# Performance work log

Hardware: AMD Instinct MI355X
Metric: run time of the kernel (lower is better)

## Reference

```python
import jax, jax.numpy as jnp
import numpy as np

EMBED = 128   # embed_dim
HEADS = 8
POINTS = 4
H_SP, W_SP = 51, 102   # hardcoded spatial_shapes in __init__
BEV = 100              # bev_res
HRES = 50              # height_res


def _make_ref_points():
    """Exact numpy replica of the spherical grid built in __init__."""
    eps = 1e-6
    x = np.linspace(-71 / 2, 71 / 2, BEV)
    y = np.linspace(-71 / 2, 71 / 2, BEV)
    z = np.linspace(-50 / 2, 50 / 2, HRES)
    gx, gy, gz = np.meshgrid(x, y, z, indexing='ij')
    phi = np.sign(gy + eps) * np.arccos(gx / (np.sqrt(gx ** 2 + gy ** 2) + eps))
    theta = np.arccos(gz / (np.sqrt(gx ** 2 + gy ** 2 + gz ** 2) + eps))
    phi = 2 * np.pi - phi
    phi[phi > 2 * np.pi] -= 2 * np.pi
    col = phi / (2 * np.pi)   # grd_col_cross
    row = theta / np.pi       # grd_row_cross
    ref = np.stack([col, row], axis=-1)              # (BEV, BEV, HRES, 2)
    ref = ref.transpose(2, 0, 1, 3).reshape(HRES, BEV * BEV, 2)
    return jnp.asarray(ref, dtype=jnp.float32)


def setup_inputs() -> dict:
    key = jax.random.key(0)
    ks = jax.random.split(key, 12)
    d = EMBED
    s = 0.02
    return {
        'query': jax.random.normal(ks[0], (1, BEV * BEV, d), jnp.float32),
        'value': jax.random.normal(ks[1], (1, H_SP * W_SP, d), jnp.float32),
        'ref_points': _make_ref_points(),
        'W_off': jax.random.normal(ks[2], (d, HEADS * POINTS * 2), jnp.float32) * s,
        'b_off': jax.random.normal(ks[3], (HEADS * POINTS * 2,), jnp.float32) * s,
        'W_attn': jax.random.normal(ks[4], (d, HEADS * POINTS), jnp.float32) * s,
        'b_attn': jax.random.normal(ks[5], (HEADS * POINTS,), jnp.float32) * s,
        'W_val': jax.random.normal(ks[6], (d, d), jnp.float32) * s,
        'b_val': jax.random.normal(ks[7], (d,), jnp.float32) * s,
        'W_out': jax.random.normal(ks[8], (d, d), jnp.float32) * s,
        'b_out': jax.random.normal(ks[9], (d,), jnp.float32) * s,
        'W_proj': jax.random.normal(ks[10], (d, 1), jnp.float32) * s,
        'b_proj': jax.random.normal(ks[11], (1,), jnp.float32) * s,
    }


def _bilinear_sample(vflat, loc):
    """grid_sample(bilinear, zero padding, align_corners=False).
    vflat: (B, H*W, hd) value maps; loc: (B, N, 2) normalized [0,1] (x,y)."""
    px = loc[..., 0] * W_SP - 0.5
    py = loc[..., 1] * H_SP - 0.5
    x0 = jnp.floor(px)
    y0 = jnp.floor(py)
    dx = (px - x0)[..., None]
    dy = (py - y0)[..., None]
    x0i = x0.astype(jnp.int32)
    y0i = y0.astype(jnp.int32)

    def gather(xi, yi):
        valid = (xi >= 0) & (xi < W_SP) & (yi >= 0) & (yi < H_SP)
        idx = jnp.clip(yi, 0, H_SP - 1) * W_SP + jnp.clip(xi, 0, W_SP - 1)
        v = jnp.take_along_axis(vflat, idx[..., None], axis=1)  # (B, N, hd)
        return v * valid[..., None].astype(vflat.dtype)

    v00 = gather(x0i, y0i)
    v01 = gather(x0i + 1, y0i)
    v10 = gather(x0i, y0i + 1)
    v11 = gather(x0i + 1, y0i + 1)
    return (v00 * (1 - dx) * (1 - dy) + v01 * dx * (1 - dy)
            + v10 * (1 - dx) * dy + v11 * dx * dy)


def reference(query, value, ref_points, W_off, b_off, W_attn, b_attn,
              W_val, b_val, W_out, b_out, W_proj, b_proj):
    bs, nq, d = query.shape
    hd = d // HEADS
    L = ref_points.shape[0]

    # query-dependent MSDA projections (identical across height levels)
    offsets = (query @ W_off + b_off).reshape(bs, nq, HEADS, POINTS, 2)
    aw = jax.nn.softmax((query @ W_attn + b_attn).reshape(bs, nq, HEADS, POINTS), axis=-1)
    awt = aw.transpose(0, 2, 1, 3)                              # (bs, heads, nq, points)
    v = (value @ W_val + b_val).reshape(bs, -1, HEADS, hd)
    vflat = v.transpose(0, 2, 1, 3).reshape(bs * HEADS, H_SP * W_SP, hd)
    norm = jnp.asarray([W_SP, H_SP], dtype=query.dtype)         # offset_normalizer [W, H]

    def per_level(ref):  # ref: (nq, 2) -> MSDA output with its internal residual
        loc = ref[None, :, None, None, :] + offsets / norm      # (bs, nq, heads, pts, 2)
        loc = loc.transpose(0, 2, 1, 3, 4).reshape(bs * HEADS, nq * POINTS, 2)
        samp = _bilinear_sample(vflat, loc).reshape(bs, HEADS, nq, POINTS, hd)
        out = jnp.einsum('bhnp,bhnpd->bnhd', awt, samp).reshape(bs, nq, d)
        return out @ W_out + b_out + query                      # mmcv MSDA adds identity

    grd = jax.vmap(per_level)(ref_points)                       # (L, bs, nq, d)
    grd_3d = grd.transpose(1, 2, 0, 3).reshape(bs, BEV, BEV, L, d)
    weights = jax.nn.softmax(grd_3d @ W_proj + b_proj, axis=3)  # (bs, BEV, BEV, L, 1)
    max_height_index = jnp.argmax(weights, axis=3)              # (bs, BEV, BEV, 1)
    grd_bev = (weights * grd_3d).sum(axis=3)                    # (bs, BEV, BEV, d)
    return grd_bev.reshape(bs, nq, d) + query, max_height_index
```

## Files before the change

### kernel.cpp

```cpp
#include <hip/hip_runtime.h>
#include <math.h>

#define EMBED   128
#define NHEADS  8
#define NPOINTS 4
#define HD      16
#define HSP     51
#define WSP     102
#define NPIX    (HSP * WSP)
#define NQ      10000
#define NLVL    50

#define GRID_A ((NPIX + 7) / 8)
#define GRID_B (NQ / 8)

__global__ __launch_bounds__(256) void k_prep(
    const float* __restrict__ value,
    const float* __restrict__ Wv,
    const float* __restrict__ bv,
    const float* __restrict__ query,
    const float* __restrict__ Woff,
    const float* __restrict__ boff,
    const float* __restrict__ Wattn,
    const float* __restrict__ battn,
    const float* __restrict__ Wout,
    const float* __restrict__ Wproj,
    float* __restrict__ vout,
    float* __restrict__ gout,
    float* __restrict__ off_out,
    float* __restrict__ aw_out) {
    const int b = blockIdx.x;
    const int t = threadIdx.x;
    __shared__ float srow[8][EMBED];
    __shared__ float4 u_s[32];

    if (b < GRID_A) {
        const int p   = t >> 5;
        const int s   = t & 31;
        const int pix = b * 8 + p;
        const int pl  = min(pix, NPIX - 1);
        *(float4*)&srow[p][s * 4] =
            *(const float4*)(value + (size_t)pl * EMBED + s * 4);
        if (t < 32) {
            float4 u4 = {0.f, 0.f, 0.f, 0.f};
            const float* w0 = Wout + (size_t)(t * 4 + 0) * EMBED;
            const float* w1 = Wout + (size_t)(t * 4 + 1) * EMBED;
            const float* w2 = Wout + (size_t)(t * 4 + 2) * EMBED;
            const float* w3 = Wout + (size_t)(t * 4 + 3) * EMBED;
#pragma unroll 4
            for (int d = 0; d < EMBED; d += 4) {
                const float4 wp = *(const float4*)(Wproj + d);
                const float4 a = *(const float4*)(w0 + d);
                const float4 c = *(const float4*)(w1 + d);
                const float4 e = *(const float4*)(w2 + d);
                const float4 f = *(const float4*)(w3 + d);
                u4.x = fmaf(a.x, wp.x, u4.x); u4.x = fmaf(a.y, wp.y, u4.x);
                u4.x = fmaf(a.z, wp.z, u4.x); u4.x = fmaf(a.w, wp.w, u4.x);
                u4.y = fmaf(c.x, wp.x, u4.y); u4.y = fmaf(c.y, wp.y, u4.y);
                u4.y = fmaf(c.z, wp.z, u4.y); u4.y = fmaf(c.w, wp.w, u4.y);
                u4.z = fmaf(e.x, wp.x, u4.z); u4.z = fmaf(e.y, wp.y, u4.z);
                u4.z = fmaf(e.z, wp.z, u4.z); u4.z = fmaf(e.w, wp.w, u4.z);
                u4.w = fmaf(f.x, wp.x, u4.w); u4.w = fmaf(f.y, wp.y, u4.w);
                u4.w = fmaf(f.z, wp.z, u4.w); u4.w = fmaf(f.w, wp.w, u4.w);
            }
            u_s[t] = u4;
        }
        __syncthreads();
        float4 acc = *(const float4*)(bv + s * 4);
        const float* vr = srow[p];
        const float* wp = Wv + s * 4;
#pragma unroll 8
        for (int k = 0; k < EMBED; ++k) {
            const float qv = vr[k];
            const float4 w4 = *(const float4*)(wp + (size_t)k * EMBED);
            acc.x = fmaf(qv, w4.x, acc.x);
            acc.y = fmaf(qv, w4.y, acc.y);
            acc.z = fmaf(qv, w4.z, acc.z);
            acc.w = fmaf(qv, w4.w, acc.w);
        }
        const float4 u4 = u_s[s];
        float gp = acc.x * u4.x;
        gp = fmaf(acc.y, u4.y, gp);
        gp = fmaf(acc.z, u4.z, gp);
        gp = fmaf(acc.w, u4.w, gp);
        gp += __shfl_xor(gp, 1, 64);
        gp += __shfl_xor(gp, 2, 64);
        if (pix < NPIX) {
            *(float4*)(vout + (size_t)pix * EMBED + s * 4) = acc;
            if ((s & 3) == 0)
                gout[(size_t)pix * NHEADS + (s >> 2)] = gp;
        }
    } else if (b < GRID_A + GRID_B) {
        const int qi = t >> 5;
        const int s  = t & 31;
        const int q  = (b - GRID_A) * 8 + qi;
        *(float4*)&srow[qi][s * 4] =
            *(const float4*)(query + (size_t)q * EMBED + s * 4);
        __syncthreads();
        if (s < 24) {
            const float* vr = srow[qi];
            const float* wp;
            int wstride;
            float4 acc;
            if (s < 16) {
                wp = Woff + s * 4; wstride = 64;
                acc = *(const float4*)(boff + s * 4);
            } else {
                wp = Wattn + (s - 16) * 4; wstride = 32;
                acc = *(const float4*)(battn + (s - 16) * 4);
            }
#pragma unroll 8
            for (int k = 0; k < EMBED; ++k) {
                const float qv = vr[k];
                const float4 w4 = *(const float4*)(wp + (size_t)k * wstride);
                acc.x = fmaf(qv, w4.x, acc.x);
                acc.y = fmaf(qv, w4.y, acc.y);
                acc.z = fmaf(qv, w4.z, acc.z);
                acc.w = fmaf(qv, w4.w, acc.w);
            }
            if (s < 16) {
                *(float4*)(off_out + (size_t)q * 64 + s * 4) = acc;
            } else {
                const float mx = fmaxf(fmaxf(acc.x, acc.y), fmaxf(acc.z, acc.w));
                const float e0 = __expf(acc.x - mx), e1 = __expf(acc.y - mx);
                const float e2 = __expf(acc.z - mx), e3 = __expf(acc.w - mx);
                const float inv = 1.f / (e0 + e1 + e2 + e3);
                float4 r;
                r.x = e0 * inv; r.y = e1 * inv; r.z = e2 * inv; r.w = e3 * inv;
                *(float4*)(aw_out + (size_t)q * 32 + (s - 16) * 4) = r;
            }
        }
    }
}

__global__ __launch_bounds__(256, 6) void k_main(
    const float* __restrict__ query,
    const float* __restrict__ refp,
    const float* __restrict__ voff,
    const float* __restrict__ vaw,
    const float* __restrict__ vflat,
    const float* __restrict__ gmap,
    const float* __restrict__ Wout,
    const float* __restrict__ bout,
    float* __restrict__ out0,
    float* __restrict__ out1) {
    const int t = threadIdx.x;
    const int qslot = t >> 7;
    const int w2 = (t >> 6) & 1;
    const int half = (t >> 5) & 1;
    const int sub = t & 31;
    const int h  = sub >> 2;
    const int c4 = sub & 3;
    const int q = blockIdx.x * 2 + qslot;

    __shared__ float  s_rpy[2][NLVL];
    __shared__ float4 s_acc[2][32];
    __shared__ float  s_z[2], s_m[2];
    __shared__ int    s_b[2];
    __shared__ float  s_e[2][2][2][13];

    if (t < 2 * NLVL) {
        const int ql = t / NLVL, l = t - ql * NLVL;
        const int qq = blockIdx.x * 2 + ql;
        s_rpy[ql][l] = refp[((size_t)l * NQ + qq) * 2 + 1];
    }

    const float4* offp = (const float4*)(voff + (size_t)q * 64 + h * 8);
    const float4 o01 = offp[0];
    const float4 o23 = offp[1];
    const float4 awv4 = *(const float4*)(vaw + (size_t)q * 32 + h * 4);
    const float rpx = refp[(size_t)q * 2];
    const float4* vbase = (const float4*)vflat + h * 4 + c4;

    const float offx[4] = {o01.x, o01.z, o23.x, o23.z};
    const float offy[4] = {o01.y, o01.w, o23.y, o23.w};
    const float awv[4]  = {awv4.x, awv4.y, awv4.z, awv4.w};

    float wx0[NPOINTS], wx1[NPOINTS], oyc[NPOINTS];
    int xo0[NPOINTS], xo1[NPOINTS];
#pragma unroll
    for (int p = 0; p < NPOINTS; ++p) {
        const float px = fmaf(rpx, (float)WSP, offx[p]) - 0.5f;
        const float fx = floorf(px);
        const float dx = px - fx;
        const int x0 = (int)fx, x1 = x0 + 1;
        const float a = awv[p];
        wx0[p] = ((unsigned)x0 < (unsigned)WSP) ? a * (1.f - dx) : 0.f;
        wx1[p] = ((unsigned)x1 < (unsigned)WSP) ? a * dx : 0.f;
        xo0[p] = min(max(x0, 0), WSP - 1) * 32;
        xo1[p] = min(max(x1, 0), WSP - 1) * 32;
        oyc[p] = offy[p] - 0.5f;
    }

    const float offx_c = (c4 == 0) ? o01.x : (c4 == 1) ? o01.z : (c4 == 2) ? o23.x : o23.z;
    const float offy_c = (c4 == 0) ? o01.y : (c4 == 1) ? o01.w : (c4 == 2) ? o23.y : o23.w;
    const float a_c    = (c4 == 0) ? awv4.x : (c4 == 1) ? awv4.y : (c4 == 2) ? awv4.z : awv4.w;
    const float pxc = fmaf(rpx, (float)WSP, offx_c) - 0.5f;
    const float fxc = floorf(pxc);
    const float dxc = pxc - fxc;
    const int x0c = (int)fxc, x1c = x0c + 1;
    const float gwx0 = ((unsigned)x0c < (unsigned)WSP) ? a_c * (1.f - dxc) : 0.f;
    const float gwx1 = ((unsigned)x1c < (unsigned)WSP) ? a_c * dxc : 0.f;
    const int gx0 = min(max(x0c, 0), WSP - 1) * NHEADS + h;
    const int gx1 = min(max(x1c, 0), WSP - 1) * NHEADS + h;
    const float oyc_c = offy_c - 0.5f;

    __syncthreads();

    const int niter = 13 - w2;
    float Z = 0.f, m = -1e30f;
    int best = 0;

#pragma unroll
    for (int i = 0; i < 13; ++i) {
        if (i >= niter) break;
        const int l = 4 * i + (w2 << 1) + half;
        const float rpy = s_rpy[qslot][l];
        const float py = fmaf(rpy, (float)HSP, oyc_c);
        const float fy = floorf(py);
        const float dy = py - fy;
        const int y0 = (int)fy, y1 = y0 + 1;
        const float t0 = ((unsigned)y0 < (unsigned)HSP) ? (1.f - dy) : 0.f;
        const float t1 = ((unsigned)y1 < (unsigned)HSP) ? dy : 0.f;
        const int r0 = min(max(y0, 0), HSP - 1) * (WSP * NHEADS);
        const int r1 = min(max(y1, 0), HSP - 1) * (WSP * NHEADS);
        const float g00 = gmap[r0 + gx0];
        const float g01 = gmap[r0 + gx1];
        const float g10 = gmap[r1 + gx0];
        const float g11 = gmap[r1 + gx1];
        float row0 = gwx0 * g00; row0 = fmaf(gwx1, g01, row0);
        float row1 = gwx0 * g10; row1 = fmaf(gwx1, g11, row1);
        float pg = t0 * row0; pg = fmaf(t1, row1, pg);
#pragma unroll
        for (int d = 1; d < 32; d <<= 1)
            pg += __shfl_xor(pg, d, 64);
        const float e = __expf(pg);
        Z += e;
        best = (pg > m) ? l : best;
        m = fmaxf(pg, m);
        if (sub == 0) s_e[qslot][w2][half][i] = e;
    }

    float4 acc = {0.f, 0.f, 0.f, 0.f};

#pragma unroll 1
    for (int i = 0; i < niter; ++i) {
        const int l = 4 * i + (w2 << 1) + half;
        const float rpy = s_rpy[qslot][l];

        float4 v00[NPOINTS], v01[NPOINTS], v10[NPOINTS], v11[NPOINTS];
        float w00[NPOINTS], w01[NPOINTS], w10[NPOINTS], w11[NPOINTS];
#pragma unroll
        for (int p = 0; p < NPOINTS; ++p) {
            const float py = fmaf(rpy, (float)HSP, oyc[p]);
            const float fy = floorf(py);
            const float dy = py - fy;
            const int y0 = (int)fy, y1 = y0 + 1;
            const float t0 = ((unsigned)y0 < (unsigned)HSP) ? (1.f - dy) : 0.f;
            const float t1 = ((unsigned)y1 < (unsigned)HSP) ? dy : 0.f;
            const int rb0 = min(max(y0, 0), HSP - 1) * (WSP * 32);
            const int rb1 = min(max(y1, 0), HSP - 1) * (WSP * 32);
            v00[p] = vbase[rb0 + xo0[p]];
            v01[p] = vbase[rb0 + xo1[p]];
            v10[p] = vbase[rb1 + xo0[p]];
            v11[p] = vbase[rb1 + xo1[p]];
            w00[p] = wx0[p] * t0;
            w01[p] = wx1[p] * t0;
            w10[p] = wx0[p] * t1;
            w11[p] = wx1[p] * t1;
        }
        float4 s = {0.f, 0.f, 0.f, 0.f};
#pragma unroll
        for (int p = 0; p < NPOINTS; ++p) {
            s.x = fmaf(w00[p], v00[p].x, s.x); s.y = fmaf(w00[p], v00[p].y, s.y);
            s.z = fmaf(w00[p], v00[p].z, s.z); s.w = fmaf(w00[p], v00[p].w, s.w);
            s.x = fmaf(w01[p], v01[p].x, s.x); s.y = fmaf(w01[p], v01[p].y, s.y);
            s.z = fmaf(w01[p], v01[p].z, s.z); s.w = fmaf(w01[p], v01[p].w, s.w);
            s.x = fmaf(w10[p], v10[p].x, s.x); s.y = fmaf(w10[p], v10[p].y, s.y);
            s.z = fmaf(w10[p], v10[p].z, s.z); s.w = fmaf(w10[p], v10[p].w, s.w);
            s.x = fmaf(w11[p], v11[p].x, s.x); s.y = fmaf(w11[p], v11[p].y, s.y);
            s.z = fmaf(w11[p], v11[p].z, s.z); s.w = fmaf(w11[p], v11[p].w, s.w);
        }
        const float e = s_e[qslot][w2][half][i];
        acc.x = fmaf(e, s.x, acc.x);
        acc.y = fmaf(e, s.y, acc.y);
        acc.z = fmaf(e, s.z, acc.z);
        acc.w = fmaf(e, s.w, acc.w);
    }

    {
        const float mo = __shfl_xor(m, 32, 64);
        const int   bo = __shfl_xor(best, 32, 64);
        const float Zo = __shfl_xor(Z, 32, 64);
        const float ax = __shfl_xor(acc.x, 32, 64);
        const float ay = __shfl_xor(acc.y, 32, 64);
        const float az = __shfl_xor(acc.z, 32, 64);
        const float aw_ = __shfl_xor(acc.w, 32, 64);
        const bool takeOther = (mo > m) || (mo == m && bo < best);
        best = takeOther ? bo : best;
        m = fmaxf(m, mo);
        Z += Zo;
        acc.x += ax; acc.y += ay; acc.z += az; acc.w += aw_;
    }

    if (w2 == 1) {
        if (half == 0) s_acc[qslot][sub] = acc;
        if ((t & 63) == 0) { s_z[qslot] = Z; s_m[qslot] = m; s_b[qslot] = best; }
    }
    __syncthreads();

    if (w2 == 0) {
        const float4 ao = s_acc[qslot][sub];
        const float Zo = s_z[qslot];
        const float mo = s_m[qslot];
        const int   bo = s_b[qslot];
        const bool takeOther = (mo > m) || (mo == m && bo < best);
        best = takeOther ? bo : best;
        Z += Zo;
        acc.x += ao.x; acc.y += ao.y; acc.z += ao.z; acc.w += ao.w;

        const float inv = 1.f / Z;
        if (half == 0) {
            float4 sv;
            sv.x = acc.x * inv; sv.y = acc.y * inv;
            sv.z = acc.z * inv; sv.w = acc.w * inv;
            s_acc[qslot][sub] = sv;
            if (sub == 0) out1[q] = (float)best;
        }

        const int dpb = sub * 4;
        float4 r = {0.f, 0.f, 0.f, 0.f};
        if (half == 0) {
            const float4 b4 = *(const float4*)(bout + dpb);
            const float4 q4 = *(const float4*)(query + (size_t)q * EMBED + dpb);
            r.x = fmaf(2.f, q4.x, b4.x);
            r.y = fmaf(2.f, q4.y, b4.y);
            r.z = fmaf(2.f, q4.z, b4.z);
            r.w = fmaf(2.f, q4.w, b4.w);
        }
        const float4* srow = s_acc[qslot];
        const int cg0 = half * 16;
#pragma unroll 4
        for (int cg = cg0; cg < cg0 + 16; ++cg) {
            const float4 s4 = srow[cg];
            const float4 w0 = *(const float4*)(Wout + (size_t)(cg * 4 + 0) * EMBED + dpb);
            const float4 w1 = *(const float4*)(Wout + (size_t)(cg * 4 + 1) * EMBED + dpb);
            const float4 w2v = *(const float4*)(Wout + (size_t)(cg * 4 + 2) * EMBED + dpb);
            const float4 w3 = *(const float4*)(Wout + (size_t)(cg * 4 + 3) * EMBED + dpb);
            r.x = fmaf(s4.x, w0.x, r.x); r.y = fmaf(s4.x, w0.y, r.y);
            r.z = fmaf(s4.x, w0.z, r.z); r.w = fmaf(s4.x, w0.w, r.w);
            r.x = fmaf(s4.y, w1.x, r.x); r.y = fmaf(s4.y, w1.y, r.y);
            r.z = fmaf(s4.y, w1.z, r.z); r.w = fmaf(s4.y, w1.w, r.w);
            r.x = fmaf(s4.z, w2v.x, r.x); r.y = fmaf(s4.z, w2v.y, r.y);
            r.z = fmaf(s4.z, w2v.z, r.z); r.w = fmaf(s4.z, w2v.w, r.w);
            r.x = fmaf(s4.w, w3.x, r.x); r.y = fmaf(s4.w, w3.y, r.y);
            r.z = fmaf(s4.w, w3.z, r.z); r.w = fmaf(s4.w, w3.w, r.w);
        }
        {
            const float rx = __shfl_xor(r.x, 32, 64);
            const float ry = __shfl_xor(r.y, 32, 64);
            const float rz = __shfl_xor(r.z, 32, 64);
            const float rw = __shfl_xor(r.w, 32, 64);
            r.x += rx; r.y += ry; r.z += rz; r.w += rw;
        }
        if (half == 0)
            *(float4*)(out0 + (size_t)q * EMBED + dpb) = r;
    }
}

extern "C" void kernel_launch(void* const* d_in, const int* in_sizes, int n_in,
                              void* d_out, int out_size, void* d_ws, size_t ws_size,
                              hipStream_t stream) {
    const float* query = (const float*)d_in[0];
    const float* value = (const float*)d_in[1];
    const float* refp  = (const float*)d_in[2];
    const float* Woff  = (const float*)d_in[3];
    const float* boff  = (const float*)d_in[4];
    const float* Wattn = (const float*)d_in[5];
    const float* battn = (const float*)d_in[6];
    const float* Wval  = (const float*)d_in[7];
    const float* bval  = (const float*)d_in[8];
    const float* Wout  = (const float*)d_in[9];
    const float* bout  = (const float*)d_in[10];
    const float* Wproj = (const float*)d_in[11];

    float* ws = (float*)d_ws;
    float* ws_v   = ws;
    float* ws_g   = ws_v + (size_t)NPIX * EMBED;
    float* ws_off = ws_g + (size_t)NPIX * NHEADS;
    float* ws_aw  = ws_off + (size_t)NQ * 64;

    float* out0 = (float*)d_out;
    float* out1 = out0 + (size_t)NQ * EMBED;

    hipLaunchKernelGGL(k_prep, dim3(GRID_A + GRID_B), dim3(256), 0, stream,
                       value, Wval, bval, query, Woff, boff, Wattn, battn,
                       Wout, Wproj, ws_v, ws_g, ws_off, ws_aw);
    hipLaunchKernelGGL(k_main, dim3(NQ / 2), dim3(256), 0, stream,
                       query, refp, ws_off, ws_aw, ws_v, ws_g, Wout, bout,
                       out0, out1);
}
```

Measured before the change: 292.7 us.

## Store projected value map in fp16 and fuse gate-logit and sampling loops

The projected value map is now written as half precision in the prep kernel and converted back to float when sampled in the main kernel, halving gather traffic and cache footprint. The separate loop that computed per-level gate logits and stored exponentials in shared memory is merged into the sampling loop, so each level's gate value and samples are computed together without a shared-memory round trip. Launch bounds occupancy hint drops from 6 to 4 blocks per SM. fp16 storage adds rounding error to sampled values.

```diff
diff --git a/kernel.cpp b/kernel.cpp
--- a/kernel.cpp
+++ b/kernel.cpp
@@ -1,4 +1,5 @@
 #include <hip/hip_runtime.h>
+#include <hip/hip_fp16.h>
 #include <math.h>
 
 #define EMBED   128
@@ -10,6 +11,15 @@
 #define NPIX    (HSP * WSP)
 #define NQ      10000
 #define NLVL    50
+
+struct h4v { __half2 a; __half2 b; };
+
+__device__ __forceinline__ float4 h4_to_f4(h4v v) {
+    const float2 lo = __half22float2(v.a);
+    const float2 hi = __half22float2(v.b);
+    float4 r; r.x = lo.x; r.y = lo.y; r.z = hi.x; r.w = hi.y;
+    return r;
+}
 
 #define GRID_A ((NPIX + 7) / 8)
 #define GRID_B (NQ / 8)
@@ -25,7 +35,7 @@
     const float* __restrict__ battn,
     const float* __restrict__ Wout,
     const float* __restrict__ Wproj,
-    float* __restrict__ vout,
+    __half* __restrict__ vout,
     float* __restrict__ gout,
     float* __restrict__ off_out,
     float* __restrict__ aw_out) {
@@ -86,7 +96,10 @@
         gp += __shfl_xor(gp, 1, 64);
         gp += __shfl_xor(gp, 2, 64);
         if (pix < NPIX) {
-            *(float4*)(vout + (size_t)pix * EMBED + s * 4) = acc;
+            h4v hv;
+            hv.a = __floats2half2_rn(acc.x, acc.y);
+            hv.b = __floats2half2_rn(acc.z, acc.w);
+            *(h4v*)(vout + (size_t)pix * EMBED + s * 4) = hv;
             if ((s & 3) == 0)
                 gout[(size_t)pix * NHEADS + (s >> 2)] = gp;
         }
@@ -133,12 +146,12 @@
     }
 }
 
-__global__ __launch_bounds__(256, 6) void k_main(
+__global__ __launch_bounds__(256, 4) void k_main(
     const float* __restrict__ query,
     const float* __restrict__ refp,
     const float* __restrict__ voff,
     const float* __restrict__ vaw,
-    const float* __restrict__ vflat,
+    const __half* __restrict__ vflat,
     const float* __restrict__ gmap,
     const float* __restrict__ Wout,
     const float* __restrict__ bout,
@@ -157,7 +170,6 @@
     __shared__ float4 s_acc[2][32];
     __shared__ float  s_z[2], s_m[2];
     __shared__ int    s_b[2];
-    __shared__ float  s_e[2][2][2][13];
 
     if (t < 2 * NLVL) {
         const int ql = t / NLVL, l = t - ql * NLVL;
@@ -170,7 +182,7 @@
     const float4 o23 = offp[1];
     const float4 awv4 = *(const float4*)(vaw + (size_t)q * 32 + h * 4);
     const float rpx = refp[(size_t)q * 2];
-    const float4* vbase = (const float4*)vflat + h * 4 + c4;
+    const h4v* vbase = (const h4v*)vflat + sub;
 
     const float offx[4] = {o01.x, o01.z, o23.x, o23.z};
     const float offy[4] = {o01.y, o01.w, o23.y, o23.w};
@@ -207,48 +219,30 @@
 
     __syncthreads();
 
-    const int niter = 13 - w2;
+    float4 acc = {0.f, 0.f, 0.f, 0.f};
     float Z = 0.f, m = -1e30f;
     int best = 0;
 
-#pragma unroll
+#pragma unroll 1
     for (int i = 0; i < 13; ++i) {
-        if (i >= niter) break;
+        if (4 * i + (w2 << 1) >= NLVL) break;
         const int l = 4 * i + (w2 << 1) + half;
         const float rpy = s_rpy[qslot][l];
-        const float py = fmaf(rpy, (float)HSP, oyc_c);
-        const float fy = floorf(py);
-        const float dy = py - fy;
-        const int y0 = (int)fy, y1 = y0 + 1;
-        const float t0 = ((unsigned)y0 < (unsigned)HSP) ? (1.f - dy) : 0.f;
-        const float t1 = ((unsigned)y1 < (unsigned)HSP) ? dy : 0.f;
-        const int r0 = min(max(y0, 0), HSP - 1) * (WSP * NHEADS);
-        const int r1 = min(max(y1, 0), HSP - 1) * (WSP * NHEADS);
-        const float g00 = gmap[r0 + gx0];
-        const float g01 = gmap[r0 + gx1];
-        const float g10 = gmap[r1 + gx0];
-        const float g11 = gmap[r1 + gx1];
-        float row0 = gwx0 * g00; row0 = fmaf(gwx1, g01, row0);
-        float row1 = gwx0 * g10; row1 = fmaf(gwx1, g11, row1);
-        float pg = t0 * row0; pg = fmaf(t1, row1, pg);
-#pragma unroll
-        for (int d = 1; d < 32; d <<= 1)
-            pg += __shfl_xor(pg, d, 64);
-        const float e = __expf(pg);
-        Z += e;
-        best = (pg > m) ? l : best;
-        m = fmaxf(pg, m);
-        if (sub == 0) s_e[qslot][w2][half][i] = e;
-    }
-
-    float4 acc = {0.f, 0.f, 0.f, 0.f};
-
-#pragma unroll 1
-    for (int i = 0; i < niter; ++i) {
-        const int l = 4 * i + (w2 << 1) + half;
-        const float rpy = s_rpy[qslot][l];
-
-        float4 v00[NPOINTS], v01[NPOINTS], v10[NPOINTS], v11[NPOINTS];
+
+        const float pyc = fmaf(rpy, (float)HSP, oyc_c);
+        const float fyc = floorf(pyc);
+        const float dyc = pyc - fyc;
+        const int gy0 = (int)fyc, gy1 = gy0 + 1;
+        const float gt0 = ((unsigned)gy0 < (unsigned)HSP) ? (1.f - dyc) : 0.f;
+        const float gt1 = ((unsigned)gy1 < (unsigned)HSP) ? dyc : 0.f;
+        const int gr0 = min(max(gy0, 0), HSP - 1) * (WSP * NHEADS);
+        const int gr1 = min(max(gy1, 0), HSP - 1) * (WSP * NHEADS);
+        const float g00 = gmap[gr0 + gx0];
+        const float g01 = gmap[gr0 + gx1];
+        const float g10 = gmap[gr1 + gx0];
+        const float g11 = gmap[gr1 + gx1];
+
+        h4v v00[NPOINTS], v01[NPOINTS], v10[NPOINTS], v11[NPOINTS];
         float w00[NPOINTS], w01[NPOINTS], w10[NPOINTS], w11[NPOINTS];
 #pragma unroll
         for (int p = 0; p < NPOINTS; ++p) {
@@ -272,20 +266,33 @@
         float4 s = {0.f, 0.f, 0.f, 0.f};
 #pragma unroll
         for (int p = 0; p < NPOINTS; ++p) {
-            s.x = fmaf(w00[p], v00[p].x, s.x); s.y = fmaf(w00[p], v00[p].y, s.y);
-            s.z = fmaf(w00[p], v00[p].z, s.z); s.w = fmaf(w00[p], v00[p].w, s.w);
-            s.x = fmaf(w01[p], v01[p].x, s.x); s.y = fmaf(w01[p], v01[p].y, s.y);
-            s.z = fmaf(w01[p], v01[p].z, s.z); s.w = fmaf(w01[p], v01[p].w, s.w);
-            s.x = fmaf(w10[p], v10[p].x, s.x); s.y = fmaf(w10[p], v10[p].y, s.y);
-            s.z = fmaf(w10[p], v10[p].z, s.z); s.w = fmaf(w10[p], v10[p].w, s.w);
-            s.x = fmaf(w11[p], v11[p].x, s.x); s.y = fmaf(w11[p], v11[p].y, s.y);
-            s.z = fmaf(w11[p], v11[p].z, s.z); s.w = fmaf(w11[p], v11[p].w, s.w);
-        }
-        const float e = s_e[qslot][w2][half][i];
+            const float4 f00 = h4_to_f4(v00[p]);
+            const float4 f01 = h4_to_f4(v01[p]);
+            const float4 f10 = h4_to_f4(v10[p]);
+            const float4 f11 = h4_to_f4(v11[p]);
+            s.x = fmaf(w00[p], f00.x, s.x); s.y = fmaf(w00[p], f00.y, s.y);
+            s.z = fmaf(w00[p], f00.z, s.z); s.w = fmaf(w00[p], f00.w, s.w);
+            s.x = fmaf(w01[p], f01.x, s.x); s.y = fmaf(w01[p], f01.y, s.y);
+            s.z = fmaf(w01[p], f01.z, s.z); s.w = fmaf(w01[p], f01.w, s.w);
+            s.x = fmaf(w10[p], f10.x, s.x); s.y = fmaf(w10[p], f10.y, s.y);
+            s.z = fmaf(w10[p], f10.z, s.z); s.w = fmaf(w10[p], f10.w, s.w);
+            s.x = fmaf(w11[p], f11.x, s.x); s.y = fmaf(w11[p], f11.y, s.y);
+            s.z = fmaf(w11[p], f11.z, s.z); s.w = fmaf(w11[p], f11.w, s.w);
+        }
+        float row0 = gwx0 * g00; row0 = fmaf(gwx1, g01, row0);
+        float row1 = gwx0 * g10; row1 = fmaf(gwx1, g11, row1);
+        float part = gt0 * row0; part = fmaf(gt1, row1, part);
+#pragma unroll
+        for (int d = 1; d < 32; d <<= 1)
+            part += __shfl_xor(part, d, 64);
+        const float e = __expf(part);
+        Z += e;
         acc.x = fmaf(e, s.x, acc.x);
         acc.y = fmaf(e, s.y, acc.y);
         acc.z = fmaf(e, s.z, acc.z);
         acc.w = fmaf(e, s.w, acc.w);
+        best = (part > m) ? l : best;
+        m = fmaxf(part, m);
     }
 
     {
@@ -385,8 +392,8 @@
     const float* Wproj = (const float*)d_in[11];
 
     float* ws = (float*)d_ws;
-    float* ws_v   = ws;
-    float* ws_g   = ws_v + (size_t)NPIX * EMBED;
+    __half* ws_v = (__half*)ws;
+    float* ws_g   = ws + (size_t)NPIX * EMBED / 2;
     float* ws_off = ws_g + (size_t)NPIX * NHEADS;
     float* ws_aw  = ws_off + (size_t)NQ * 64;
 
```

After: 286.3 us. -2.2%, faster.
